# Kernel optimization log

Measured on AMD Instinct MI355X. Metric: run time of the kernel, lower is better.

## Reference

```python
import jax, jax.numpy as jnp
import numpy as np

IN_DIM = 256
OUT_DIM = 256

def setup_inputs() -> dict:
    key = jax.random.key(0)
    k1, k2, k3, k4 = jax.random.split(key, 4)
    B, N, K, D = 4, 10000, 16, IN_DIM
    x = jax.random.normal(k1, (B, N, D), dtype=jnp.float32)
    neigh = jax.random.randint(k2, (N, K), 0, N, dtype=jnp.int64)
    # nn.Linear(2*in_dim, out_dim): W [out, 2*in], b [out]
    bound = 1.0 / np.sqrt(2 * D)
    W = jax.random.uniform(k3, (OUT_DIM, 2 * D), minval=-bound, maxval=bound, dtype=jnp.float32)
    b = jax.random.uniform(k4, (OUT_DIM,), minval=-bound, maxval=bound, dtype=jnp.float32)
    return {"x": x, "neigh": neigh, "W": W, "b": b}

def reference(x, neigh, W, b):
    # x: [B,N,D], neigh: [N,K] with -1 = padding
    mask = (neigh >= 0)                                # [N,K]
    idx = jnp.clip(neigh, 0, None)                     # [N,K]
    # batch_gather_nodes: x_nei[b,n,k,:] = x[b, idx[n,k], :]
    x_nei = x[:, idx, :]                               # [B,N,K,D]
    x_nei = x_nei * mask[None, :, :, None].astype(x.dtype)
    denom = jnp.clip(mask.sum(axis=1), 1, None).astype(x.dtype)  # [N]
    agg = x_nei.sum(axis=2) / denom[None, :, None]     # [B,N,D]
    h = jnp.concatenate([x, agg], axis=-1)             # [B,N,2D]
    return jax.nn.relu(jnp.einsum('bnd,od->bno', h, W) + b)
```

## Files before the change

### kernel.cpp

```cpp
#include <hip/hip_runtime.h>
#include <hip/hip_bf16.h>
#include <stdint.h>

#define B_   4
#define N_   10000
#define K_   16
#define D_   256
#define OUT_ 256
#define M_   (B_ * N_)
#define CW   32
#define NCH  8
#define CHUNK_ELEMS ((size_t)N_ * B_ * CW)

typedef __attribute__((ext_vector_type(8))) short          short8;
typedef __attribute__((ext_vector_type(8))) unsigned short ushort8;
typedef __attribute__((ext_vector_type(4))) float          f32x4;
typedef __attribute__((ext_vector_type(4))) unsigned short ushort4_t;

__device__ inline unsigned short f2bf(float f) {
    __hip_bfloat16 h = __float2bfloat16(f);
    return *reinterpret_cast<unsigned short*>(&h);
}
__device__ inline float bf2f(unsigned short u) {
    unsigned int v = ((unsigned int)u) << 16;
    return __builtin_bit_cast(float, v);
}

__global__ __launch_bounds__(256) void wprep(const float* __restrict__ W,
                                             unsigned short* __restrict__ Wb) {
    const int g  = blockIdx.x * 256 + threadIdx.x;
    const int op = g >> 6;
    const int k0 = (g & 63) * 4;
    const float* src = (op < OUT_) ? (W + (size_t)op * 512 + k0)
                                   : (W + (size_t)(op - OUT_) * 512 + 256 + k0);
    const float4 v = *(const float4*)src;
    ushort4_t s;
    s.x = f2bf(v.x); s.y = f2bf(v.y); s.z = f2bf(v.z); s.w = f2bf(v.w);
    *(ushort4_t*)(Wb + (size_t)op * 256 + k0) = s;
}

__global__ __launch_bounds__(256) void gemm_fused(const float* __restrict__ x,
                                                  const unsigned short* __restrict__ Wb,
                                                  float* __restrict__ y1,
                                                  unsigned short* __restrict__ y2c) {
    __shared__ unsigned short As[64 * 32];
    __shared__ unsigned short Bs[256 * 32];

    const int tid    = threadIdx.x;
    const int w      = tid >> 6;
    const int lane   = tid & 63;
    const int q      = lane >> 4;
    const int r16    = lane & 15;
    const int half   = blockIdx.x & 1;
    const int tile_m = (blockIdx.x >> 1) * 64;

    const int crow = lane >> 2;
    const int kofs = (lane & 3) * 8;

    const int arow  = tid >> 2;
    const int acol8 = (tid & 3) * 8;
    const float* xrow = x + (size_t)(tile_m + arow) * D_ + acol8;

    const unsigned short* bsrc =
        Wb + ((size_t)(half * OUT_ + w * 64 + crow)) * D_ + kofs;

    f32x4 acc[4][4] = {};

    float4 va0 = *(const float4*)(xrow);
    float4 va1 = *(const float4*)(xrow + 4);

    for (int kk = 0; kk < D_; kk += 32) {
#pragma unroll
        for (int t = 0; t < 4; ++t) {
            __builtin_amdgcn_global_load_lds(
                (const __attribute__((address_space(1))) void*)(bsrc + (size_t)t * 16 * D_ + kk),
                (__attribute__((address_space(3))) void*)(Bs + (w * 4 + t) * 512),
                16, 0, 0);
        }
        ushort8 s;
        s[0] = f2bf(va0.x); s[1] = f2bf(va0.y); s[2] = f2bf(va0.z); s[3] = f2bf(va0.w);
        s[4] = f2bf(va1.x); s[5] = f2bf(va1.y); s[6] = f2bf(va1.z); s[7] = f2bf(va1.w);
        *(ushort8*)(As + arow * 32 + acol8) = s;
        if (kk + 32 < D_) {
            va0 = *(const float4*)(xrow + kk + 32);
            va1 = *(const float4*)(xrow + kk + 36);
        }
        __syncthreads();

        short8 a[4], bf[4];
#pragma unroll
        for (int i = 0; i < 4; ++i)
            a[i] = *(const short8*)(As + (i * 16 + r16) * 32 + q * 8);
#pragma unroll
        for (int j = 0; j < 4; ++j)
            bf[j] = *(const short8*)(Bs + (w * 64 + j * 16 + r16) * 32 + q * 8);

#pragma unroll
        for (int i = 0; i < 4; ++i)
#pragma unroll
            for (int j = 0; j < 4; ++j)
                acc[i][j] = __builtin_amdgcn_mfma_f32_16x16x32_bf16(a[i], bf[j], acc[i][j], 0, 0, 0);

        __syncthreads();
    }

    if (half == 0) {
#pragma unroll
        for (int i = 0; i < 4; ++i) {
#pragma unroll
            for (int reg = 0; reg < 4; ++reg) {
                const int m = tile_m + i * 16 + q * 4 + reg;
                float* row = y1 + (size_t)m * OUT_ + w * 64;
#pragma unroll
                for (int j = 0; j < 4; ++j)
                    row[j * 16 + r16] = acc[i][j][reg];
            }
        }
    } else {
#pragma unroll
        for (int i = 0; i < 4; ++i) {
#pragma unroll
            for (int reg = 0; reg < 4; ++reg) {
                const int m = tile_m + i * 16 + q * 4 + reg;
                const int b = (m >= N_) + (m >= 2 * N_) + (m >= 3 * N_);
                const int n = m - b * N_;
                unsigned short* rbase = y2c + (size_t)(n * B_ + b) * CW;
#pragma unroll
                for (int j = 0; j < 4; ++j) {
                    const int o2 = w * 64 + j * 16 + r16;
                    rbase[(size_t)(o2 >> 5) * CHUNK_ELEMS + (o2 & 31)] =
                        f2bf(acc[i][j][reg]);
                }
            }
        }
    }
}

__global__ __launch_bounds__(256) void gather_out(const unsigned short* __restrict__ y2c,
                                                  const float* __restrict__ y1,
                                                  const int*   __restrict__ neigh,
                                                  const float* __restrict__ bias,
                                                  float* __restrict__ out) {
    const int c   = blockIdx.x & 7;
    const int g   = blockIdx.x >> 3;
    const int n0  = g * 16;
    const int tid = threadIdx.x;

    __shared__ int   idx_s[16 * K_];
    __shared__ float inv_s[16];

    idx_s[tid] = neigh[n0 * K_ + tid];
    __syncthreads();
    if (tid < 16) {
        int cnt = 0;
#pragma unroll
        for (int k = 0; k < K_; ++k) cnt += idx_s[tid * K_ + k] >= 0 ? 1 : 0;
        inv_s[tid] = 1.0f / (float)(cnt > 1 ? cnt : 1);
    }
    __syncthreads();

    const int q  = tid & 3;
    const int tl = tid >> 2;
    const int ns = tl >> 2;
    const int b  = tl & 3;

    const unsigned short* ycc = y2c + (size_t)c * CHUNK_ELEMS;

    int jj[K_];
#pragma unroll
    for (int k = 0; k < K_; ++k) jj[k] = idx_s[ns * K_ + k];

    ushort8 vv[K_];
#pragma unroll
    for (int k = 0; k < K_; ++k) {
        const int jc = jj[k] >= 0 ? jj[k] : 0;
        vv[k] = *(const ushort8*)(ycc + ((size_t)jc * B_ + b) * CW + q * 8);
    }

    const size_t mo = (size_t)(b * N_ + n0 + ns) * OUT_ + c * CW + q * 8;
    const f32x4 s0 = *(const f32x4*)(y1 + mo);
    const f32x4 s1 = *(const f32x4*)(y1 + mo + 4);
    const f32x4 b0 = *(const f32x4*)(bias + c * CW + q * 8);
    const f32x4 b1 = *(const f32x4*)(bias + c * CW + q * 8 + 4);

    float acc[8] = {0.f, 0.f, 0.f, 0.f, 0.f, 0.f, 0.f, 0.f};
#pragma unroll
    for (int k = 0; k < K_; ++k) {
        const float m = jj[k] >= 0 ? 1.f : 0.f;
#pragma unroll
        for (int e = 0; e < 8; ++e) acc[e] += bf2f(vv[k][e]) * m;
    }
    const float inv = inv_s[ns];

    f32x4 o0, o1;
#pragma unroll
    for (int e = 0; e < 4; ++e) {
        float v0 = acc[e] * inv + s0[e] + b0[e];
        float v1 = acc[e + 4] * inv + s1[e] + b1[e];
        o0[e] = v0 > 0.f ? v0 : 0.f;
        o1[e] = v1 > 0.f ? v1 : 0.f;
    }
    __builtin_nontemporal_store(o0, (f32x4*)(out + mo));
    __builtin_nontemporal_store(o1, (f32x4*)(out + mo + 4));
}

extern "C" void kernel_launch(void* const* d_in, const int* in_sizes, int n_in,
                              void* d_out, int out_size, void* d_ws, size_t ws_size,
                              hipStream_t stream) {
    const float* x     = (const float*)d_in[0];
    const int*   neigh = (const int*)d_in[1];
    const float* W     = (const float*)d_in[2];
    const float* bias  = (const float*)d_in[3];
    float*       out   = (float*)d_out;

    unsigned short* Wb  = (unsigned short*)d_ws;
    float*          y1  = (float*)(Wb + 512 * D_);
    unsigned short* y2c = (unsigned short*)(y1 + (size_t)M_ * OUT_);

    wprep<<<128, 256, 0, stream>>>(W, Wb);
    gemm_fused<<<(M_ / 64) * 2, 256, 0, stream>>>(x, Wb, y1, y2c);
    gather_out<<<(N_ / 16) * NCH, 256, 0, stream>>>(y2c, y1, neigh, bias, out);
}
```

Before: 144.3 us.

## Restructure GEMM to keep a weight quarter resident in LDS with direct A-register loads

The weight prep now writes W into a blocked layout so that each GEMM block can load a full 128-column quarter of the bf16 weights into LDS once. The GEMM tiles 128 rows per block with four N-quarters per tile, and blocks are mapped so that tiles are spread across the eight XCDs. A operands are read straight from global memory into registers with a three-deep prefetch, which removes the per-k-step LDS staging of A and the barriers inside the loop. The cost is that x is read four times instead of twice, LDS use is large (64KB per block), and the last tile needs bounds checks.

Result: slower. 156.3 us (+8.3%).

```diff
diff --git a/kernel.cpp b/kernel.cpp
--- a/kernel.cpp
+++ b/kernel.cpp
@@ -11,6 +11,8 @@
 #define CW   32
 #define NCH  8
 #define CHUNK_ELEMS ((size_t)N_ * B_ * CW)
+#define MT_  313
+#define QSZ  32768
 
 typedef __attribute__((ext_vector_type(8))) short          short8;
 typedef __attribute__((ext_vector_type(8))) unsigned short ushort8;
@@ -28,108 +30,128 @@
 
 __global__ __launch_bounds__(256) void wprep(const float* __restrict__ W,
                                              unsigned short* __restrict__ Wb) {
-    const int g  = blockIdx.x * 256 + threadIdx.x;
-    const int op = g >> 6;
-    const int k0 = (g & 63) * 4;
-    const float* src = (op < OUT_) ? (W + (size_t)op * 512 + k0)
-                                   : (W + (size_t)(op - OUT_) * 512 + 256 + k0);
+    const int g    = blockIdx.x * 256 + threadIdx.x;
+    const int orow = g >> 6;
+    const int k0   = (g & 63) * 4;
+    const float* src = (orow < OUT_) ? (W + (size_t)orow * 512 + k0)
+                                     : (W + (size_t)(orow - OUT_) * 512 + 256 + k0);
     const float4 v = *(const float4*)src;
     ushort4_t s;
     s.x = f2bf(v.x); s.y = f2bf(v.y); s.z = f2bf(v.z); s.w = f2bf(v.w);
-    *(ushort4_t*)(Wb + (size_t)op * 256 + k0) = s;
-}
-
-__global__ __launch_bounds__(256) void gemm_fused(const float* __restrict__ x,
-                                                  const unsigned short* __restrict__ Wb,
-                                                  float* __restrict__ y1,
-                                                  unsigned short* __restrict__ y2c) {
-    __shared__ unsigned short As[64 * 32];
-    __shared__ unsigned short Bs[256 * 32];
-
-    const int tid    = threadIdx.x;
-    const int w      = tid >> 6;
-    const int lane   = tid & 63;
-    const int q      = lane >> 4;
-    const int r16    = lane & 15;
-    const int half   = blockIdx.x & 1;
-    const int tile_m = (blockIdx.x >> 1) * 64;
-
-    const int crow = lane >> 2;
-    const int kofs = (lane & 3) * 8;
-
-    const int arow  = tid >> 2;
-    const int acol8 = (tid & 3) * 8;
-    const float* xrow = x + (size_t)(tile_m + arow) * D_ + acol8;
-
-    const unsigned short* bsrc =
-        Wb + ((size_t)(half * OUT_ + w * 64 + crow)) * D_ + kofs;
-
-    f32x4 acc[4][4] = {};
-
-    float4 va0 = *(const float4*)(xrow);
-    float4 va1 = *(const float4*)(xrow + 4);
-
-    for (int kk = 0; kk < D_; kk += 32) {
-#pragma unroll
-        for (int t = 0; t < 4; ++t) {
+    const size_t off = (size_t)(((orow >> 7) * 8 + (k0 >> 5)) * 128 + (orow & 127)) * 32
+                     + (k0 & 31);
+    *(ushort4_t*)(Wb + off) = s;
+}
+
+__global__ __launch_bounds__(256) void gemm_res(const float* __restrict__ x,
+                                                const unsigned short* __restrict__ Wb,
+                                                float* __restrict__ y1,
+                                                unsigned short* __restrict__ y2c) {
+    __shared__ unsigned short Bs[8 * 128 * 32];
+
+    const int tid  = threadIdx.x;
+    const int w    = tid >> 6;
+    const int lane = tid & 63;
+    const int q    = lane >> 4;
+    const int r16  = lane & 15;
+
+    const int bi  = blockIdx.x;
+    const int xcd = bi & 7;
+    const int jj  = bi >> 3;
+    const int g   = (jj >> 2) * 8 + xcd;
+    const int qtr = jj & 3;
+    if (g >= MT_) return;
+    const int tile_m = g * 128;
+
+    {
+        const unsigned short* wsrc = Wb + (size_t)qtr * QSZ + w * 512 + lane * 8;
+        unsigned short*       ldst = Bs + w * 512;
+#pragma unroll
+        for (int it = 0; it < 16; ++it) {
             __builtin_amdgcn_global_load_lds(
-                (const __attribute__((address_space(1))) void*)(bsrc + (size_t)t * 16 * D_ + kk),
-                (__attribute__((address_space(3))) void*)(Bs + (w * 4 + t) * 512),
+                (const __attribute__((address_space(1))) void*)(wsrc + it * 2048),
+                (__attribute__((address_space(3))) void*)(ldst + it * 2048),
                 16, 0, 0);
         }
-        ushort8 s;
-        s[0] = f2bf(va0.x); s[1] = f2bf(va0.y); s[2] = f2bf(va0.z); s[3] = f2bf(va0.w);
-        s[4] = f2bf(va1.x); s[5] = f2bf(va1.y); s[6] = f2bf(va1.z); s[7] = f2bf(va1.w);
-        *(ushort8*)(As + arow * 32 + acol8) = s;
-        if (kk + 32 < D_) {
-            va0 = *(const float4*)(xrow + kk + 32);
-            va1 = *(const float4*)(xrow + kk + 36);
-        }
-        __syncthreads();
-
-        short8 a[4], bf[4];
-#pragma unroll
-        for (int i = 0; i < 4; ++i)
-            a[i] = *(const short8*)(As + (i * 16 + r16) * 32 + q * 8);
-#pragma unroll
-        for (int j = 0; j < 4; ++j)
-            bf[j] = *(const short8*)(Bs + (w * 64 + j * 16 + r16) * 32 + q * 8);
-
-#pragma unroll
-        for (int i = 0; i < 4; ++i)
-#pragma unroll
-            for (int j = 0; j < 4; ++j)
-                acc[i][j] = __builtin_amdgcn_mfma_f32_16x16x32_bf16(a[i], bf[j], acc[i][j], 0, 0, 0);
-
-        __syncthreads();
-    }
-
-    if (half == 0) {
-#pragma unroll
-        for (int i = 0; i < 4; ++i) {
+    }
+    __syncthreads();
+
+    int r0 = tile_m + w * 32 + r16;
+    int r1 = r0 + 16;
+    if (r0 > M_ - 1) r0 = M_ - 1;
+    if (r1 > M_ - 1) r1 = M_ - 1;
+    const float* ap0 = x + (size_t)r0 * D_ + q * 8;
+    const float* ap1 = x + (size_t)r1 * D_ + q * 8;
+
+    f32x4 acc[2][8] = {};
+
+    float4 A0[3], A1[3], A2[3], A3[3];
+#pragma unroll
+    for (int s = 0; s < 3; ++s) {
+        A0[s] = *(const float4*)(ap0 + s * 32);
+        A1[s] = *(const float4*)(ap0 + s * 32 + 4);
+        A2[s] = *(const float4*)(ap1 + s * 32);
+        A3[s] = *(const float4*)(ap1 + s * 32 + 4);
+    }
+
+#pragma unroll
+    for (int ks = 0; ks < 8; ++ks) {
+        const int sl = ks % 3;
+        short8 a0, a1;
+        a0[0] = (short)f2bf(A0[sl].x); a0[1] = (short)f2bf(A0[sl].y);
+        a0[2] = (short)f2bf(A0[sl].z); a0[3] = (short)f2bf(A0[sl].w);
+        a0[4] = (short)f2bf(A1[sl].x); a0[5] = (short)f2bf(A1[sl].y);
+        a0[6] = (short)f2bf(A1[sl].z); a0[7] = (short)f2bf(A1[sl].w);
+        a1[0] = (short)f2bf(A2[sl].x); a1[1] = (short)f2bf(A2[sl].y);
+        a1[2] = (short)f2bf(A2[sl].z); a1[3] = (short)f2bf(A2[sl].w);
+        a1[4] = (short)f2bf(A3[sl].x); a1[5] = (short)f2bf(A3[sl].y);
+        a1[6] = (short)f2bf(A3[sl].z); a1[7] = (short)f2bf(A3[sl].w);
+        if (ks + 3 < 8) {
+            A0[sl] = *(const float4*)(ap0 + (ks + 3) * 32);
+            A1[sl] = *(const float4*)(ap0 + (ks + 3) * 32 + 4);
+            A2[sl] = *(const float4*)(ap1 + (ks + 3) * 32);
+            A3[sl] = *(const float4*)(ap1 + (ks + 3) * 32 + 4);
+        }
+        const unsigned short* bbase = Bs + ks * 4096 + r16 * 32 + q * 8;
+#pragma unroll
+        for (int j = 0; j < 8; ++j) {
+            const short8 b = *(const short8*)(bbase + j * 512);
+            acc[0][j] = __builtin_amdgcn_mfma_f32_16x16x32_bf16(a0, b, acc[0][j], 0, 0, 0);
+            acc[1][j] = __builtin_amdgcn_mfma_f32_16x16x32_bf16(a1, b, acc[1][j], 0, 0, 0);
+        }
+    }
+
+    if (qtr < 2) {
+#pragma unroll
+        for (int i = 0; i < 2; ++i) {
 #pragma unroll
             for (int reg = 0; reg < 4; ++reg) {
-                const int m = tile_m + i * 16 + q * 4 + reg;
-                float* row = y1 + (size_t)m * OUT_ + w * 64;
-#pragma unroll
-                for (int j = 0; j < 4; ++j)
-                    row[j * 16 + r16] = acc[i][j][reg];
+                const int m = tile_m + w * 32 + i * 16 + q * 4 + reg;
+                if (m < M_) {
+                    float* row = y1 + (size_t)m * OUT_ + qtr * 128;
+#pragma unroll
+                    for (int j = 0; j < 8; ++j)
+                        row[j * 16 + r16] = acc[i][j][reg];
+                }
             }
         }
     } else {
-#pragma unroll
-        for (int i = 0; i < 4; ++i) {
+        const int cbase = (qtr - 2) * 4;
+#pragma unroll
+        for (int i = 0; i < 2; ++i) {
 #pragma unroll
             for (int reg = 0; reg < 4; ++reg) {
-                const int m = tile_m + i * 16 + q * 4 + reg;
-                const int b = (m >= N_) + (m >= 2 * N_) + (m >= 3 * N_);
-                const int n = m - b * N_;
-                unsigned short* rbase = y2c + (size_t)(n * B_ + b) * CW;
-#pragma unroll
-                for (int j = 0; j < 4; ++j) {
-                    const int o2 = w * 64 + j * 16 + r16;
-                    rbase[(size_t)(o2 >> 5) * CHUNK_ELEMS + (o2 & 31)] =
-                        f2bf(acc[i][j][reg]);
+                const int m = tile_m + w * 32 + i * 16 + q * 4 + reg;
+                if (m < M_) {
+                    const int b = (m >= N_) + (m >= 2 * N_) + (m >= 3 * N_);
+                    const int n = m - b * N_;
+                    unsigned short* rb = y2c + (size_t)(n * B_ + b) * CW;
+#pragma unroll
+                    for (int j = 0; j < 8; ++j) {
+                        const int c   = cbase + (j >> 1);
+                        const int col = (j & 1) * 16 + r16;
+                        rb[(size_t)c * CHUNK_ELEMS + col] = f2bf(acc[i][j][reg]);
+                    }
                 }
             }
         }
@@ -218,6 +240,6 @@
     unsigned short* y2c = (unsigned short*)(y1 + (size_t)M_ * OUT_);
 
     wprep<<<128, 256, 0, stream>>>(W, Wb);
-    gemm_fused<<<(M_ / 64) * 2, 256, 0, stream>>>(x, Wb, y1, y2c);
+    gemm_res<<<(((MT_ + 7) / 8) * 8) * 4, 256, 0, stream>>>(x, Wb, y1, y2c);
     gather_out<<<(N_ / 16) * NCH, 256, 0, stream>>>(y2c, y1, neigh, bias, out);
 }
```

## Rewrite GEMM with 512-thread blocks, swizzled LDS, K=64 steps and XCD-aware tile mapping

Applied to the files above, without the earlier changes.

The weight prep now writes bf16 weights in a pre-swizzled, K-sliced layout, so the GEMM can copy whole 64-wide K slices straight into LDS with contiguous global_load_lds and read them back with XOR-swizzled addresses that avoid bank conflicts. The GEMM uses 8 waves arranged 2x4 over a 64x256 tile and K steps of 64, which halves the number of barriers. Block indices are remapped so that tiles are spread across the XCDs. For the y2 half, the MFMA operands are swapped so each lane holds four consecutive output columns, letting the bf16 stores go out as 8-byte vectors instead of scalar stores. The cost is more LDS per block, which may lower occupancy, and some padded blocks that exit early.

After: 140.7 us. -2.5%, faster.

```diff
diff --git a/kernel.cpp b/kernel.cpp
--- a/kernel.cpp
+++ b/kernel.cpp
@@ -11,6 +11,8 @@
 #define CW   32
 #define NCH  8
 #define CHUNK_ELEMS ((size_t)N_ * B_ * CW)
+#define TILES_ 625
+#define TPH    16384
 
 typedef __attribute__((ext_vector_type(8))) short          short8;
 typedef __attribute__((ext_vector_type(8))) unsigned short ushort8;
@@ -29,88 +31,132 @@
 __global__ __launch_bounds__(256) void wprep(const float* __restrict__ W,
                                              unsigned short* __restrict__ Wb) {
     const int g  = blockIdx.x * 256 + threadIdx.x;
-    const int op = g >> 6;
-    const int k0 = (g & 63) * 4;
-    const float* src = (op < OUT_) ? (W + (size_t)op * 512 + k0)
-                                   : (W + (size_t)(op - OUT_) * 512 + 256 + k0);
-    const float4 v = *(const float4*)src;
+    const int h  = g >> 14;
+    const int t  = g & 16383;
+    const int ks = t >> 12;
+    const int rr = (t >> 4) & 255;
+    const int kg = (t & 15) * 4;
+    const float4 v = *(const float4*)(W + (size_t)rr * 512 + h * 256 + ks * 64 + kg);
     ushort4_t s;
     s.x = f2bf(v.x); s.y = f2bf(v.y); s.z = f2bf(v.z); s.w = f2bf(v.w);
-    *(ushort4_t*)(Wb + (size_t)op * 256 + k0) = s;
-}
-
-__global__ __launch_bounds__(256) void gemm_fused(const float* __restrict__ x,
-                                                  const unsigned short* __restrict__ Wb,
-                                                  float* __restrict__ y1,
-                                                  unsigned short* __restrict__ y2c) {
-    __shared__ unsigned short As[64 * 32];
-    __shared__ unsigned short Bs[256 * 32];
-
-    const int tid    = threadIdx.x;
-    const int w      = tid >> 6;
-    const int lane   = tid & 63;
-    const int q      = lane >> 4;
-    const int r16    = lane & 15;
-    const int half   = blockIdx.x & 1;
-    const int tile_m = (blockIdx.x >> 1) * 64;
-
-    const int crow = lane >> 2;
-    const int kofs = (lane & 3) * 8;
-
-    const int arow  = tid >> 2;
-    const int acol8 = (tid & 3) * 8;
-    const float* xrow = x + (size_t)(tile_m + arow) * D_ + acol8;
-
-    const unsigned short* bsrc =
-        Wb + ((size_t)(half * OUT_ + w * 64 + crow)) * D_ + kofs;
-
-    f32x4 acc[4][4] = {};
-
-    float4 va0 = *(const float4*)(xrow);
-    float4 va1 = *(const float4*)(xrow + 4);
-
-    for (int kk = 0; kk < D_; kk += 32) {
-#pragma unroll
-        for (int t = 0; t < 4; ++t) {
-            __builtin_amdgcn_global_load_lds(
-                (const __attribute__((address_space(1))) void*)(bsrc + (size_t)t * 16 * D_ + kk),
-                (__attribute__((address_space(3))) void*)(Bs + (w * 4 + t) * 512),
-                16, 0, 0);
-        }
+    const int off = ((rr * 128 + kg * 2) ^ ((rr & 7) << 4)) >> 1;
+    *(ushort4_t*)(Wb + (size_t)(h * 4 + ks) * TPH + off) = s;
+}
+
+__global__ __launch_bounds__(512) void gemm3(const float* __restrict__ x,
+                                             const unsigned short* __restrict__ Wb,
+                                             float* __restrict__ y1,
+                                             unsigned short* __restrict__ y2c) {
+    __shared__ unsigned short As[64 * 64];
+    __shared__ unsigned short Bs[256 * 64];
+
+    const int tid  = threadIdx.x;
+    const int w    = tid >> 6;
+    const int lane = tid & 63;
+    const int q    = lane >> 4;
+    const int r16  = lane & 15;
+    const int wm   = w >> 2;
+    const int wn   = w & 3;
+
+    const int bi   = blockIdx.x;
+    const int xcd  = bi & 7;
+    const int u    = bi >> 3;
+    const int g    = (u >> 1) * 8 + xcd;
+    const int half = u & 1;
+    if (g >= TILES_) return;
+    const int tile_m = g * 64;
+
+    const int arow = tid >> 3;
+    const int akg  = (tid & 7) * 8;
+    const float* ap = x + (size_t)(tile_m + arow) * D_ + akg;
+    const unsigned int awoff = (unsigned)((arow * 128 + akg * 2) ^ ((arow & 7) << 4));
+
+    const unsigned short* wsrc0 = Wb + (size_t)(half * 4) * TPH + tid * 8;
+
+    const unsigned int sw = (unsigned)((r16 & 7) << 4);
+
+    f32x4 acc[2][4] = {};
+
+    float4 c0 = *(const float4*)ap;
+    float4 c1 = *(const float4*)(ap + 4);
+#pragma unroll
+    for (int i2 = 0; i2 < 4; ++i2) {
+        __builtin_amdgcn_global_load_lds(
+            (const __attribute__((address_space(1))) void*)(wsrc0 + i2 * 4096),
+            (__attribute__((address_space(3))) void*)(Bs + tid * 8 + i2 * 4096),
+            16, 0, 0);
+    }
+    {
         ushort8 s;
-        s[0] = f2bf(va0.x); s[1] = f2bf(va0.y); s[2] = f2bf(va0.z); s[3] = f2bf(va0.w);
-        s[4] = f2bf(va1.x); s[5] = f2bf(va1.y); s[6] = f2bf(va1.z); s[7] = f2bf(va1.w);
-        *(ushort8*)(As + arow * 32 + acol8) = s;
-        if (kk + 32 < D_) {
-            va0 = *(const float4*)(xrow + kk + 32);
-            va1 = *(const float4*)(xrow + kk + 36);
-        }
-        __syncthreads();
-
-        short8 a[4], bf[4];
-#pragma unroll
-        for (int i = 0; i < 4; ++i)
-            a[i] = *(const short8*)(As + (i * 16 + r16) * 32 + q * 8);
-#pragma unroll
-        for (int j = 0; j < 4; ++j)
-            bf[j] = *(const short8*)(Bs + (w * 64 + j * 16 + r16) * 32 + q * 8);
-
-#pragma unroll
-        for (int i = 0; i < 4; ++i)
-#pragma unroll
-            for (int j = 0; j < 4; ++j)
-                acc[i][j] = __builtin_amdgcn_mfma_f32_16x16x32_bf16(a[i], bf[j], acc[i][j], 0, 0, 0);
-
-        __syncthreads();
+        s[0] = f2bf(c0.x); s[1] = f2bf(c0.y); s[2] = f2bf(c0.z); s[3] = f2bf(c0.w);
+        s[4] = f2bf(c1.x); s[5] = f2bf(c1.y); s[6] = f2bf(c1.z); s[7] = f2bf(c1.w);
+        *(ushort8*)((char*)As + awoff) = s;
+    }
+    __syncthreads();
+
+#pragma unroll
+    for (int ks = 0; ks < 4; ++ks) {
+        float4 n0, n1;
+        if (ks < 3) {
+            n0 = *(const float4*)(ap + (ks + 1) * 64);
+            n1 = *(const float4*)(ap + (ks + 1) * 64 + 4);
+        }
+
+#pragma unroll
+        for (int ksub = 0; ksub < 2; ++ksub) {
+            short8 a[2], bf[4];
+#pragma unroll
+            for (int i = 0; i < 2; ++i) {
+                const unsigned int ad =
+                    (unsigned)((wm * 32 + i * 16 + r16) * 128 + ksub * 64 + q * 16) ^ sw;
+                a[i] = *(const short8*)((const char*)As + ad);
+            }
+#pragma unroll
+            for (int j = 0; j < 4; ++j) {
+                const unsigned int bd =
+                    (unsigned)((wn * 64 + j * 16 + r16) * 128 + ksub * 64 + q * 16) ^ sw;
+                bf[j] = *(const short8*)((const char*)Bs + bd);
+            }
+            if (half == 0) {
+#pragma unroll
+                for (int i = 0; i < 2; ++i)
+#pragma unroll
+                    for (int j = 0; j < 4; ++j)
+                        acc[i][j] = __builtin_amdgcn_mfma_f32_16x16x32_bf16(a[i], bf[j], acc[i][j], 0, 0, 0);
+            } else {
+#pragma unroll
+                for (int i = 0; i < 2; ++i)
+#pragma unroll
+                    for (int j = 0; j < 4; ++j)
+                        acc[i][j] = __builtin_amdgcn_mfma_f32_16x16x32_bf16(bf[j], a[i], acc[i][j], 0, 0, 0);
+            }
+        }
+
+        if (ks < 3) {
+            __syncthreads();
+            const unsigned short* wsrc = wsrc0 + (size_t)(ks + 1) * TPH;
+#pragma unroll
+            for (int i2 = 0; i2 < 4; ++i2) {
+                __builtin_amdgcn_global_load_lds(
+                    (const __attribute__((address_space(1))) void*)(wsrc + i2 * 4096),
+                    (__attribute__((address_space(3))) void*)(Bs + tid * 8 + i2 * 4096),
+                    16, 0, 0);
+            }
+            ushort8 s;
+            s[0] = f2bf(n0.x); s[1] = f2bf(n0.y); s[2] = f2bf(n0.z); s[3] = f2bf(n0.w);
+            s[4] = f2bf(n1.x); s[5] = f2bf(n1.y); s[6] = f2bf(n1.z); s[7] = f2bf(n1.w);
+            *(ushort8*)((char*)As + awoff) = s;
+            __syncthreads();
+        }
     }
 
     if (half == 0) {
 #pragma unroll
-        for (int i = 0; i < 4; ++i) {
+        for (int i = 0; i < 2; ++i) {
 #pragma unroll
             for (int reg = 0; reg < 4; ++reg) {
-                const int m = tile_m + i * 16 + q * 4 + reg;
-                float* row = y1 + (size_t)m * OUT_ + w * 64;
+                const int m = tile_m + wm * 32 + i * 16 + q * 4 + reg;
+                float* row = y1 + (size_t)m * OUT_ + wn * 64;
 #pragma unroll
                 for (int j = 0; j < 4; ++j)
                     row[j * 16 + r16] = acc[i][j][reg];
@@ -118,19 +164,20 @@
         }
     } else {
 #pragma unroll
-        for (int i = 0; i < 4; ++i) {
-#pragma unroll
-            for (int reg = 0; reg < 4; ++reg) {
-                const int m = tile_m + i * 16 + q * 4 + reg;
-                const int b = (m >= N_) + (m >= 2 * N_) + (m >= 3 * N_);
-                const int n = m - b * N_;
-                unsigned short* rbase = y2c + (size_t)(n * B_ + b) * CW;
-#pragma unroll
-                for (int j = 0; j < 4; ++j) {
-                    const int o2 = w * 64 + j * 16 + r16;
-                    rbase[(size_t)(o2 >> 5) * CHUNK_ELEMS + (o2 & 31)] =
-                        f2bf(acc[i][j][reg]);
-                }
+        for (int i = 0; i < 2; ++i) {
+            const int m  = tile_m + wm * 32 + i * 16 + r16;
+            const int bb = (m >= N_) + (m >= 2 * N_) + (m >= 3 * N_);
+            const int n  = m - bb * N_;
+            unsigned short* rb = y2c + (size_t)(n * B_ + bb) * CW;
+#pragma unroll
+            for (int j = 0; j < 4; ++j) {
+                const int o2  = wn * 64 + j * 16 + q * 4;
+                const int cch = o2 >> 5;
+                const int col = o2 & 31;
+                ushort4_t p;
+                p.x = f2bf(acc[i][j][0]); p.y = f2bf(acc[i][j][1]);
+                p.z = f2bf(acc[i][j][2]); p.w = f2bf(acc[i][j][3]);
+                *(ushort4_t*)(rb + (size_t)cch * CHUNK_ELEMS + col) = p;
             }
         }
     }
@@ -214,10 +261,10 @@
     float*       out   = (float*)d_out;
 
     unsigned short* Wb  = (unsigned short*)d_ws;
-    float*          y1  = (float*)(Wb + 512 * D_);
+    float*          y1  = (float*)(Wb + 8 * TPH);
     unsigned short* y2c = (unsigned short*)(y1 + (size_t)M_ * OUT_);
 
     wprep<<<128, 256, 0, stream>>>(W, Wb);
-    gemm_fused<<<(M_ / 64) * 2, 256, 0, stream>>>(x, Wb, y1, y2c);
+    gemm3<<<158 * 8, 256 * 2, 0, stream>>>(x, Wb, y1, y2c);
     gather_out<<<(N_ / 16) * NCH, 256, 0, stream>>>(y2c, y1, neigh, bias, out);
 }
```

## Shrink GEMM M-tile to 32, XCD-aware block mapping, transposed MFMA for packed y2 stores

Applied to the files above, without the earlier changes.

The GEMM row tile drops from 64 to 32 rows. Block indices are remapped so that the two output halves of consecutive tiles fall on the same XCD. For the neighbour-projection half, the MFMA operands are swapped so each lane holds four consecutive output columns, which lets it write 4-wide bf16 vector stores instead of scalar ones. The gather kernel now reads y1 with nontemporal loads. This trades more blocks and extra reloading of W against better load balance and write coalescing.

New measurement: 143.0 us. About the same (-0.9%).

```diff
diff --git a/kernel.cpp b/kernel.cpp
--- a/kernel.cpp
+++ b/kernel.cpp
@@ -7,10 +7,12 @@
 #define K_   16
 #define D_   256
 #define OUT_ 256
+#define KDIM 512
 #define M_   (B_ * N_)
 #define CW   32
 #define NCH  8
-#define CHUNK_ELEMS ((size_t)N_ * B_ * CW)
+#define CHUNK_ELEMS ((size_t)M_ * CW)
+#define T32_ 1250
 
 typedef __attribute__((ext_vector_type(8))) short          short8;
 typedef __attribute__((ext_vector_type(8))) unsigned short ushort8;
@@ -39,74 +41,83 @@
     *(ushort4_t*)(Wb + (size_t)op * 256 + k0) = s;
 }
 
-__global__ __launch_bounds__(256) void gemm_fused(const float* __restrict__ x,
-                                                  const unsigned short* __restrict__ Wb,
-                                                  float* __restrict__ y1,
-                                                  unsigned short* __restrict__ y2c) {
-    __shared__ unsigned short As[64 * 32];
+__global__ __launch_bounds__(256) void gemm32(const float* __restrict__ x,
+                                              const unsigned short* __restrict__ Wb,
+                                              float* __restrict__ y1,
+                                              unsigned short* __restrict__ y2c) {
+    __shared__ unsigned short As[32 * 32];
     __shared__ unsigned short Bs[256 * 32];
 
-    const int tid    = threadIdx.x;
-    const int w      = tid >> 6;
-    const int lane   = tid & 63;
-    const int q      = lane >> 4;
-    const int r16    = lane & 15;
-    const int half   = blockIdx.x & 1;
-    const int tile_m = (blockIdx.x >> 1) * 64;
+    const int tid  = threadIdx.x;
+    const int w    = tid >> 6;
+    const int lane = tid & 63;
+    const int q    = lane >> 4;
+    const int r16  = lane & 15;
+
+    const int bi   = blockIdx.x;
+    const int xcd  = bi & 7;
+    const int u    = bi >> 3;
+    const int g    = (u >> 1) * 8 + xcd;
+    const int half = u & 1;
+    if (g >= T32_) return;
+    const int tile_m = g * 32;
+
+    const int arow  = tid >> 3;
+    const int acol4 = (tid & 7) * 4;
+    const float* xrow = x + (size_t)(tile_m + arow) * D_ + acol4;
 
     const int crow = lane >> 2;
     const int kofs = (lane & 3) * 8;
-
-    const int arow  = tid >> 2;
-    const int acol8 = (tid & 3) * 8;
-    const float* xrow = x + (size_t)(tile_m + arow) * D_ + acol8;
-
     const unsigned short* bsrc =
-        Wb + ((size_t)(half * OUT_ + w * 64 + crow)) * D_ + kofs;
-
-    f32x4 acc[4][4] = {};
-
-    float4 va0 = *(const float4*)(xrow);
-    float4 va1 = *(const float4*)(xrow + 4);
+        Wb + ((size_t)(half * OUT_) + crow) * D_ + kofs;
+
+    f32x4 acc[2][4] = {};
+
+    float4 va = *(const float4*)(xrow);
 
     for (int kk = 0; kk < D_; kk += 32) {
 #pragma unroll
         for (int t = 0; t < 4; ++t) {
+            const int c = w * 4 + t;
             __builtin_amdgcn_global_load_lds(
-                (const __attribute__((address_space(1))) void*)(bsrc + (size_t)t * 16 * D_ + kk),
-                (__attribute__((address_space(3))) void*)(Bs + (w * 4 + t) * 512),
+                (const __attribute__((address_space(1))) void*)(bsrc + (size_t)c * 16 * D_ + kk),
+                (__attribute__((address_space(3))) void*)(Bs + c * 512),
                 16, 0, 0);
         }
-        ushort8 s;
-        s[0] = f2bf(va0.x); s[1] = f2bf(va0.y); s[2] = f2bf(va0.z); s[3] = f2bf(va0.w);
-        s[4] = f2bf(va1.x); s[5] = f2bf(va1.y); s[6] = f2bf(va1.z); s[7] = f2bf(va1.w);
-        *(ushort8*)(As + arow * 32 + acol8) = s;
-        if (kk + 32 < D_) {
-            va0 = *(const float4*)(xrow + kk + 32);
-            va1 = *(const float4*)(xrow + kk + 36);
-        }
+        ushort4_t s;
+        s.x = f2bf(va.x); s.y = f2bf(va.y); s.z = f2bf(va.z); s.w = f2bf(va.w);
+        *(ushort4_t*)(As + arow * 32 + acol4) = s;
+        if (kk + 32 < D_) va = *(const float4*)(xrow + kk + 32);
         __syncthreads();
 
-        short8 a[4], bf[4];
-#pragma unroll
-        for (int i = 0; i < 4; ++i)
+        short8 a[2], bf[4];
+#pragma unroll
+        for (int i = 0; i < 2; ++i)
             a[i] = *(const short8*)(As + (i * 16 + r16) * 32 + q * 8);
 #pragma unroll
         for (int j = 0; j < 4; ++j)
             bf[j] = *(const short8*)(Bs + (w * 64 + j * 16 + r16) * 32 + q * 8);
 
-#pragma unroll
-        for (int i = 0; i < 4; ++i)
-#pragma unroll
-            for (int j = 0; j < 4; ++j)
-                acc[i][j] = __builtin_amdgcn_mfma_f32_16x16x32_bf16(a[i], bf[j], acc[i][j], 0, 0, 0);
+        if (half == 0) {
+#pragma unroll
+            for (int i = 0; i < 2; ++i)
+#pragma unroll
+                for (int j = 0; j < 4; ++j)
+                    acc[i][j] = __builtin_amdgcn_mfma_f32_16x16x32_bf16(a[i], bf[j], acc[i][j], 0, 0, 0);
+        } else {
+#pragma unroll
+            for (int i = 0; i < 2; ++i)
+#pragma unroll
+                for (int j = 0; j < 4; ++j)
+                    acc[i][j] = __builtin_amdgcn_mfma_f32_16x16x32_bf16(bf[j], a[i], acc[i][j], 0, 0, 0);
+        }
 
         __syncthreads();
     }
 
     if (half == 0) {
 #pragma unroll
-        for (int i = 0; i < 4; ++i) {
+        for (int i = 0; i < 2; ++i) {
 #pragma unroll
             for (int reg = 0; reg < 4; ++reg) {
                 const int m = tile_m + i * 16 + q * 4 + reg;
@@ -118,19 +129,20 @@
         }
     } else {
 #pragma unroll
-        for (int i = 0; i < 4; ++i) {
-#pragma unroll
-            for (int reg = 0; reg < 4; ++reg) {
-                const int m = tile_m + i * 16 + q * 4 + reg;
-                const int b = (m >= N_) + (m >= 2 * N_) + (m >= 3 * N_);
-                const int n = m - b * N_;
-                unsigned short* rbase = y2c + (size_t)(n * B_ + b) * CW;
-#pragma unroll
-                for (int j = 0; j < 4; ++j) {
-                    const int o2 = w * 64 + j * 16 + r16;
-                    rbase[(size_t)(o2 >> 5) * CHUNK_ELEMS + (o2 & 31)] =
-                        f2bf(acc[i][j][reg]);
-                }
+        for (int i = 0; i < 2; ++i) {
+            const int m  = tile_m + i * 16 + r16;
+            const int bb = (m >= N_) + (m >= 2 * N_) + (m >= 3 * N_);
+            const int n  = m - bb * N_;
+            unsigned short* rb = y2c + (size_t)(n * B_ + bb) * CW;
+#pragma unroll
+            for (int j = 0; j < 4; ++j) {
+                const int o2  = w * 64 + j * 16 + q * 4;
+                const int cch = o2 >> 5;
+                const int col = o2 & 31;
+                ushort4_t p;
+                p.x = f2bf(acc[i][j][0]); p.y = f2bf(acc[i][j][1]);
+                p.z = f2bf(acc[i][j][2]); p.w = f2bf(acc[i][j][3]);
+                *(ushort4_t*)(rb + (size_t)cch * CHUNK_ELEMS + col) = p;
             }
         }
     }
@@ -178,8 +190,8 @@
     }
 
     const size_t mo = (size_t)(b * N_ + n0 + ns) * OUT_ + c * CW + q * 8;
-    const f32x4 s0 = *(const f32x4*)(y1 + mo);
-    const f32x4 s1 = *(const f32x4*)(y1 + mo + 4);
+    const f32x4 s0 = __builtin_nontemporal_load((const f32x4*)(y1 + mo));
+    const f32x4 s1 = __builtin_nontemporal_load((const f32x4*)(y1 + mo + 4));
     const f32x4 b0 = *(const f32x4*)(bias + c * CW + q * 8);
     const f32x4 b1 = *(const f32x4*)(bias + c * CW + q * 8 + 4);
 
@@ -218,6 +230,6 @@
     unsigned short* y2c = (unsigned short*)(y1 + (size_t)M_ * OUT_);
 
     wprep<<<128, 256, 0, stream>>>(W, Wb);
-    gemm_fused<<<(M_ / 64) * 2, 256, 0, stream>>>(x, Wb, y1, y2c);
+    gemm32<<<157 * 8 * 2, 256, 0, stream>>>(x, Wb, y1, y2c);
     gather_out<<<(N_ / 16) * NCH, 256, 0, stream>>>(y2c, y1, neigh, bias, out);
 }
```
